# Kernel tuning notes

Hardware: AMD Instinct MI355X
Metric: run time of the kernel (lower is better)

Reference implementation:

```python
import jax, jax.numpy as jnp
import numpy as np

B, T, K = 512, 1024, 48


def setup_inputs() -> dict:
    key = jax.random.key(0)
    k1, k2, k3, k4, k5, k6 = jax.random.split(key, 6)
    return {
        "emission_scores": jax.random.normal(k1, (B, T, K), dtype=jnp.float32),
        "lengths": jax.random.randint(k2, (B,), 1, T + 1, dtype=jnp.int64),
        "tags": jax.random.randint(k3, (B, T), 0, K, dtype=jnp.int64),
        "prior": 0.1 * jax.random.normal(k4, (K,), dtype=jnp.float32),
        "transition": 0.1 * jax.random.normal(k5, (K, K), dtype=jnp.float32),
        "final_transition": 0.1 * jax.random.normal(k6, (K,), dtype=jnp.float32),
    }


def _partition_function(emission_scores, lengths, prior, transition, final_transition):
    batch, timesteps, num_tags = emission_scores.shape
    # alpha_0[b, i] = emis[b, 0, i] + prior[i]
    alpha0 = emission_scores[:, 0, :] + prior[None, :]

    def step(prev_alpha, emis_t):
        # alpha_t[b, i] = logsumexp_j(prev_alpha[b, j] + transition[i, j]) + emis_t[b, i]
        a = jax.nn.logsumexp(prev_alpha[:, None, :] + transition[None, :, :], axis=2)
        a = a + emis_t
        return a, a

    emis_rest = jnp.swapaxes(emission_scores, 0, 1)[1:]  # [T-1, B, K]
    _, alphas = jax.lax.scan(step, alpha0, emis_rest)
    alphas = jnp.concatenate([alpha0[None], alphas], axis=0)  # [T, B, K]
    alpha_final = alphas[lengths - 1, jnp.arange(batch)]  # [B, K] at last valid step
    alpha_final = alpha_final + final_transition[None, :]
    return jax.nn.logsumexp(alpha_final, axis=1)


def _score_path(emission_scores, lengths, tags, prior, transition, final_transition):
    batch, timesteps, num_tags = emission_scores.shape
    emis_tag = jnp.take_along_axis(emission_scores, tags[:, :, None], axis=2)[..., 0]  # [B, T]
    trans = transition[tags[:, 1:], tags[:, :-1]]  # [B, T-1]
    pr = prior[tags[:, 0]][:, None]  # [B, 1]
    scores = jnp.concatenate([pr, trans], axis=1) + emis_tag  # [B, T]
    valid = jnp.arange(timesteps)[None, :] < lengths[:, None]  # True for t < length
    scores = jnp.where(valid, scores, 0.0)
    final_tags = tags[jnp.arange(batch), lengths - 1]
    return jnp.sum(scores, axis=1) + final_transition[final_tags]


def reference(emission_scores, lengths, tags, prior, transition, final_transition):
    lengths = jnp.clip(lengths, 1, None)
    logZ = _partition_function(emission_scores, lengths, prior, transition, final_transition)
    path = _score_path(emission_scores, lengths, tags, prior, transition, final_transition)
    return jnp.mean(logZ - path)
```

## Files before the change

### kernel.cpp

```cpp
#include <hip/hip_runtime.h>


#define BB    512
#define TT    1024
#define KK    48
#define GG    16
#define NGRP  32
#define NSLOT 16
#define SLOTB 4096
#define PHASE 8
#define NPROD 4
#define BLKT  (64 * (1 + NPROD))

typedef __attribute__((ext_vector_type(4))) short bf16x4;
typedef __attribute__((ext_vector_type(4))) float f32x4;

__device__ __forceinline__ f32x4 mfma16(bf16x4 a, bf16x4 b, f32x4 c) {
#if __has_builtin(__builtin_amdgcn_mfma_f32_16x16x16bf16_1k)
    return __builtin_amdgcn_mfma_f32_16x16x16bf16_1k(a, b, c, 0, 0, 0);
#else
    f32x4 d;
    asm volatile("v_mfma_f32_16x16x16_bf16 %0, %1, %2, %3"
                 : "=v"(d) : "v"(a), "v"(b), "v"(c));
    return d;
#endif
}

__device__ __forceinline__ unsigned pk2(float lo, float hi) {
    return __builtin_amdgcn_perm(__float_as_uint(hi) + 0x8000u,
                                 __float_as_uint(lo) + 0x8000u,
                                 0x07060302u);
}
__device__ __forceinline__ bf16x4 pack4(float a, float b, float c, float d) {
    union { unsigned u[2]; bf16x4 v; } x;
    x.u[0] = pk2(a, b);
    x.u[1] = pk2(c, d);
    return x.v;
}

__device__ __forceinline__ float wave_reduce_sum(float v) {
    #pragma unroll
    for (int off = 32; off > 0; off >>= 1)
        v += __shfl_xor(v, off, 64);
    return v;
}

__device__ __forceinline__ void load_lds16(const float* g, void* l) {
    __builtin_amdgcn_global_load_lds(
        (const __attribute__((address_space(1))) unsigned int*)g,
        (__attribute__((address_space(3))) unsigned int*)l,
        16, 0, 0);
}

__global__ __launch_bounds__(BLKT, 1) void crf_main_kernel(
    const float* __restrict__ emis,
    const int*   __restrict__ lengths,
    const int*   __restrict__ tags,
    const float* __restrict__ prior,
    const float* __restrict__ trans,
    const float* __restrict__ finalT,
    float*       __restrict__ ws)
{
    __shared__ __align__(16) unsigned char ring[NSLOT * SLOTB];

    const int tid  = threadIdx.x;
    const int wv   = tid >> 6;
    const int lane = tid & 63;

    if (blockIdx.x >= NGRP) {
        const int b = blockIdx.x - NGRP;
        int len = lengths[b];
        len = (len < 1) ? 1 : (len > TT ? TT : len);
        const float* eb = emis + (size_t)b * TT * KK;
        const int*   tg = tags + (size_t)b * TT;
        float ps = 0.0f;
        for (int t = tid; t < len; t += BLKT) {
            int cur = tg[t];
            float ev = eb[(size_t)t * KK + cur];
            float tr = (t == 0) ? prior[cur] : trans[cur * KK + tg[t - 1]];
            ps += ev + tr;
        }
        ps = wave_reduce_sum(ps);
        float* red = (float*)ring;
        if (lane == 0) red[wv] = ps;
        __syncthreads();
        if (tid == 0) {
            float s = red[0];
            #pragma unroll
            for (int j = 1; j <= NPROD; ++j) s += red[j];
            ws[BB + b] = s + finalT[tg[len - 1]];
        }
        return;
    }

    const int g = blockIdx.x;

    int myLen = lengths[g * GG + (lane & 15)];
    myLen = (myLen < 1) ? 1 : (myLen > TT ? TT : myLen);
    int gmax = myLen;
    #pragma unroll
    for (int off = 32; off > 0; off >>= 1) {
        int o = __shfl_xor(gmax, off, 64);
        gmax = (o > gmax) ? o : gmax;
    }
    const int nsteps = gmax - 1;
    const int nphase = (nsteps + PHASE - 1) / PHASE;

    if (wv >= 1) {
        const float* base[4];
        #pragma unroll
        for (int j = 0; j < 4; ++j) {
            int s  = j * 4 + (lane >> 4);
            int kg = (lane & 15) ^ s;
            if (kg >= 12) kg = 0;
            base[j] = emis + ((size_t)(g * GG + s) * TT) * KK + kg * 4;
        }
        for (int k = 0; k < nphase; ++k) {
            int t0 = 1 + k * PHASE + (wv - 1);
            #pragma unroll
            for (int h = 0; h < 2; ++h) {
                int t  = t0 + 4 * h;
                int tc = (t > nsteps) ? nsteps : t;
                unsigned char* lp = &ring[(t & (NSLOT - 1)) * SLOTB];
                #pragma unroll
                for (int j = 0; j < 4; ++j)
                    load_lds16(base[j] + (size_t)tc * KK, lp + j * 1024);
            }
            __syncthreads();
        }
        return;
    }

    const int col   = lane & 15;
    const int grp   = lane >> 4;
    const int rbase = grp * 4;
    const int seq   = g * GG + col;
    const int lenn1 = myLen - 1;

    bf16x4 A[3][3];
    #pragma unroll
    for (int mt = 0; mt < 3; ++mt) {
        #pragma unroll
        for (int kt = 0; kt < 3; ++kt) {
            float4 tv = *reinterpret_cast<const float4*>(
                trans + (size_t)(mt * 16 + col) * KK + kt * 16 + rbase);
            A[mt][kt] = pack4(__expf(tv.x), __expf(tv.y),
                              __expf(tv.z), __expf(tv.w));
        }
    }

    float expF[12];
    #pragma unroll
    for (int mt = 0; mt < 3; ++mt) {
        float4 fv = *reinterpret_cast<const float4*>(finalT + mt * 16 + rbase);
        expF[mt*4+0] = __expf(fv.x); expF[mt*4+1] = __expf(fv.y);
        expF[mt*4+2] = __expf(fv.z); expF[mt*4+3] = __expf(fv.w);
    }

    const float* ebase = emis + (size_t)seq * TT * KK + rbase;

    float w[12];
    float c;
    float zcap = 0.0f;
    {
        float a0[12];
        #pragma unroll
        for (int mt = 0; mt < 3; ++mt) {
            float4 ev = *reinterpret_cast<const float4*>(ebase + mt * 16);
            float4 pv = *reinterpret_cast<const float4*>(prior + mt * 16 + rbase);
            a0[mt*4+0] = ev.x + pv.x;
            a0[mt*4+1] = ev.y + pv.y;
            a0[mt*4+2] = ev.z + pv.z;
            a0[mt*4+3] = ev.w + pv.w;
        }
        float mx = a0[0];
        #pragma unroll
        for (int r = 1; r < 12; ++r) mx = fmaxf(mx, a0[r]);
        mx = fmaxf(mx, __shfl_xor(mx, 16, 64));
        mx = fmaxf(mx, __shfl_xor(mx, 32, 64));
        c = mx;
        #pragma unroll
        for (int r = 0; r < 12; ++r) w[r] = __expf(a0[r] - c);
        if (__ballot(lenn1 == 0)) {
            float S = 0.0f;
            #pragma unroll
            for (int r = 0; r < 12; ++r) S = fmaf(w[r], expF[r], S);
            S += __shfl_xor(S, 16, 64);
            S += __shfl_xor(S, 32, 64);
            if (lenn1 == 0) zcap = c + __logf(S);
        }
    }

    bf16x4 Bt[3];
    Bt[0] = pack4(w[0], w[1], w[2],  w[3]);
    Bt[1] = pack4(w[4], w[5], w[6],  w[7]);
    Bt[2] = pack4(w[8], w[9], w[10], w[11]);

    int loff[3];
    #pragma unroll
    for (int mt = 0; mt < 3; ++mt)
        loff[mt] = col * 256 + (((mt * 4 + grp) ^ col) << 4);

    const f32x4 zero4 = {0.f, 0.f, 0.f, 0.f};
    for (int k = 0; k < nphase; ++k) {
        __syncthreads();
        #pragma unroll
        for (int s8 = 0; s8 < PHASE; ++s8) {
            const int t = 1 + k * PHASE + s8;
            const unsigned char* sp = &ring[(t & (NSLOT - 1)) * SLOTB];
            float4 E0 = *reinterpret_cast<const float4*>(sp + loff[0]);
            float4 E1 = *reinterpret_cast<const float4*>(sp + loff[1]);
            float4 E2 = *reinterpret_cast<const float4*>(sp + loff[2]);

            f32x4 D0 = mfma16(A[0][0], Bt[0], zero4);
            f32x4 D1 = mfma16(A[1][0], Bt[0], zero4);
            f32x4 D2 = mfma16(A[2][0], Bt[0], zero4);
            D0 = mfma16(A[0][1], Bt[1], D0);
            D1 = mfma16(A[1][1], Bt[1], D1);
            D2 = mfma16(A[2][1], Bt[1], D2);
            D0 = mfma16(A[0][2], Bt[2], D0);
            D1 = mfma16(A[1][2], Bt[2], D1);
            D2 = mfma16(A[2][2], Bt[2], D2);

            w[0]  = D0.x * __expf(E0.x);
            w[1]  = D0.y * __expf(E0.y);
            w[2]  = D0.z * __expf(E0.z);
            w[3]  = D0.w * __expf(E0.w);
            w[4]  = D1.x * __expf(E1.x);
            w[5]  = D1.y * __expf(E1.y);
            w[6]  = D1.z * __expf(E1.z);
            w[7]  = D1.w * __expf(E1.w);
            w[8]  = D2.x * __expf(E2.x);
            w[9]  = D2.y * __expf(E2.y);
            w[10] = D2.z * __expf(E2.z);
            w[11] = D2.w * __expf(E2.w);

            if ((t & 7) == 0) {
                float mx = w[0];
                #pragma unroll
                for (int r = 1; r < 12; ++r) mx = fmaxf(mx, w[r]);
                mx = fmaxf(mx, __shfl_xor(mx, 16, 64));
                mx = fmaxf(mx, __shfl_xor(mx, 32, 64));
                c += __logf(mx);
                float rm = __builtin_amdgcn_rcpf(mx);
                #pragma unroll
                for (int r = 0; r < 12; ++r) w[r] *= rm;
            }

            if (__ballot(t == lenn1)) {
                float S = 0.0f;
                #pragma unroll
                for (int r = 0; r < 12; ++r) S = fmaf(w[r], expF[r], S);
                S += __shfl_xor(S, 16, 64);
                S += __shfl_xor(S, 32, 64);
                if (t == lenn1) zcap = c + __logf(S);
            }

            Bt[0] = pack4(w[0], w[1], w[2],  w[3]);
            Bt[1] = pack4(w[4], w[5], w[6],  w[7]);
            Bt[2] = pack4(w[8], w[9], w[10], w[11]);
        }
    }

    if (lane < GG) ws[seq] = zcap;
}

__global__ __launch_bounds__(512) void reduce_mean_kernel(
    const float* __restrict__ ws, float* __restrict__ out)
{
    __shared__ float sm[8];
    int tid = threadIdx.x;
    float x = ws[tid] - ws[BB + tid];
    x = wave_reduce_sum(x);
    if ((tid & 63) == 0) sm[tid >> 6] = x;
    __syncthreads();
    if (tid < 8) {
        float y = sm[tid];
        y += __shfl_xor(y, 1, 64);
        y += __shfl_xor(y, 2, 64);
        y += __shfl_xor(y, 4, 64);
        if (tid == 0) out[0] = y * (1.0f / 512.0f);
    }
}

extern "C" void kernel_launch(void* const* d_in, const int* in_sizes, int n_in,
                              void* d_out, int out_size, void* d_ws, size_t ws_size,
                              hipStream_t stream) {
    const float* emis    = (const float*)d_in[0];
    const int*   lengths = (const int*)  d_in[1];
    const int*   tags    = (const int*)  d_in[2];
    const float* prior   = (const float*)d_in[3];
    const float* trans   = (const float*)d_in[4];
    const float* finalT  = (const float*)d_in[5];

    float* ws  = (float*)d_ws;
    float* out = (float*)d_out;

    crf_main_kernel<<<NGRP + BB, BLKT, 0, stream>>>(emis, lengths, tags, prior,
                                                    trans, finalT, ws);
    reduce_mean_kernel<<<1, 512, 0, stream>>>(ws, out);
}
```

Before: 341.2 us.

## Replace barrier-synced LDS ring with flag-based producer/consumer and producer-side exp

Producer waves now load emissions into registers, apply exp, and write the pre-exponentiated values into a compact LDS ring. Block-wide __syncthreads is replaced by per-producer and consumer counters in LDS polled with s_sleep, so the serial consumer wave no longer waits at barriers. The consumer's per-step exp work moves to the producers. Producers drop from 4 to 3 and bf16 packing uses the hardware cvt_pk_bf16 builtin where available. The cost is spin-wait polling and correctness that depends on LDS memory ordering without barriers.

Measured after the change: 331.6 us. 1.03x faster.

```diff
diff --git a/kernel.cpp b/kernel.cpp
--- a/kernel.cpp
+++ b/kernel.cpp
@@ -7,10 +7,10 @@
 #define GG    16
 #define NGRP  32
 #define NSLOT 16
-#define SLOTB 4096
+#define SLOTB (KK * GG * 4)
 #define PHASE 8
-#define NPROD 4
-#define BLKT  (64 * (1 + NPROD))
+#define NPROD 3
+#define BLKT  256
 
 typedef __attribute__((ext_vector_type(4))) short bf16x4;
 typedef __attribute__((ext_vector_type(4))) float f32x4;
@@ -26,11 +26,20 @@
 #endif
 }
 
+#if __has_builtin(__builtin_amdgcn_cvt_pk_bf16_f32)
+typedef __attribute__((ext_vector_type(2))) __bf16 bf16x2_v;
+__device__ __forceinline__ unsigned pk2(float lo, float hi) {
+    union { bf16x2_v v; unsigned u; } x;
+    x.v = __builtin_amdgcn_cvt_pk_bf16_f32(lo, hi);
+    return x.u;
+}
+#else
 __device__ __forceinline__ unsigned pk2(float lo, float hi) {
     return __builtin_amdgcn_perm(__float_as_uint(hi) + 0x8000u,
                                  __float_as_uint(lo) + 0x8000u,
                                  0x07060302u);
 }
+#endif
 __device__ __forceinline__ bf16x4 pack4(float a, float b, float c, float d) {
     union { unsigned u[2]; bf16x4 v; } x;
     x.u[0] = pk2(a, b);
@@ -43,13 +52,6 @@
     for (int off = 32; off > 0; off >>= 1)
         v += __shfl_xor(v, off, 64);
     return v;
-}
-
-__device__ __forceinline__ void load_lds16(const float* g, void* l) {
-    __builtin_amdgcn_global_load_lds(
-        (const __attribute__((address_space(1))) unsigned int*)g,
-        (__attribute__((address_space(3))) unsigned int*)l,
-        16, 0, 0);
 }
 
 __global__ __launch_bounds__(BLKT, 1) void crf_main_kernel(
@@ -62,6 +64,8 @@
     float*       __restrict__ ws)
 {
     __shared__ __align__(16) unsigned char ring[NSLOT * SLOTB];
+    __shared__ int prodCnt[NPROD];
+    __shared__ int consCnt;
 
     const int tid  = threadIdx.x;
     const int wv   = tid >> 6;
@@ -84,16 +88,17 @@
         float* red = (float*)ring;
         if (lane == 0) red[wv] = ps;
         __syncthreads();
-        if (tid == 0) {
-            float s = red[0];
-            #pragma unroll
-            for (int j = 1; j <= NPROD; ++j) s += red[j];
-            ws[BB + b] = s + finalT[tg[len - 1]];
-        }
+        if (tid == 0)
+            ws[BB + b] = red[0] + red[1] + red[2] + red[3] + finalT[tg[len - 1]];
         return;
     }
 
     const int g = blockIdx.x;
+
+    if (tid == 0) {
+        prodCnt[0] = 0; prodCnt[1] = 0; prodCnt[2] = 0; consCnt = 0;
+    }
+    __syncthreads();
 
     int myLen = lengths[g * GG + (lane & 15)];
     myLen = (myLen < 1) ? 1 : (myLen > TT ? TT : myLen);
@@ -107,27 +112,60 @@
     const int nphase = (nsteps + PHASE - 1) / PHASE;
 
     if (wv >= 1) {
-        const float* base[4];
-        #pragma unroll
-        for (int j = 0; j < 4; ++j) {
-            int s  = j * 4 + (lane >> 4);
-            int kg = (lane & 15) ^ s;
-            if (kg >= 12) kg = 0;
-            base[j] = emis + ((size_t)(g * GG + s) * TT) * KK + kg * 4;
-        }
+        size_t go[3]; int lo16[3];
+        #pragma unroll
+        for (int j = 0; j < 3; ++j) {
+            int idx = lane + 64 * j;
+            int s   = idx / 12;
+            int kg  = idx - s * 12;
+            go[j]   = (size_t)(g * GG + s) * (TT * KK) + kg * 4;
+            lo16[j] = idx * 16;
+        }
+        const int sA = wv - 1;
+        float4 L[9];
+
+#define PLOAD(KP)                                                          \
+        {                                                                  \
+            _Pragma("unroll")                                              \
+            for (int h = 0; h < 3; ++h) {                                  \
+                int s = sA + 3 * h;                                        \
+                if (s < PHASE) {                                           \
+                    int t  = 1 + (KP) * PHASE + s;                         \
+                    int tc = (t > nsteps) ? nsteps : t;                    \
+                    _Pragma("unroll")                                      \
+                    for (int j = 0; j < 3; ++j)                            \
+                        L[h*3+j] = *reinterpret_cast<const float4*>(       \
+                            emis + go[j] + (size_t)tc * KK);               \
+                }                                                          \
+            }                                                              \
+        }
+
+        PLOAD(0);
+        volatile int* vc = &consCnt;
         for (int k = 0; k < nphase; ++k) {
-            int t0 = 1 + k * PHASE + (wv - 1);
+            while (*vc < k - 1) __builtin_amdgcn_s_sleep(1);
+            asm volatile("" ::: "memory");
             #pragma unroll
-            for (int h = 0; h < 2; ++h) {
-                int t  = t0 + 4 * h;
-                int tc = (t > nsteps) ? nsteps : t;
-                unsigned char* lp = &ring[(t & (NSLOT - 1)) * SLOTB];
-                #pragma unroll
-                for (int j = 0; j < 4; ++j)
-                    load_lds16(base[j] + (size_t)tc * KK, lp + j * 1024);
+            for (int h = 0; h < 3; ++h) {
+                int s = sA + 3 * h;
+                if (s < PHASE) {
+                    int t = 1 + k * PHASE + s;
+                    unsigned char* bp = &ring[(t & (NSLOT - 1)) * SLOTB];
+                    #pragma unroll
+                    for (int j = 0; j < 3; ++j) {
+                        float4 l = L[h*3+j];
+                        float4 e;
+                        e.x = __expf(l.x); e.y = __expf(l.y);
+                        e.z = __expf(l.z); e.w = __expf(l.w);
+                        *reinterpret_cast<float4*>(bp + lo16[j]) = e;
+                    }
+                }
             }
-            __syncthreads();
-        }
+            __threadfence_block();
+            if (lane == 0) *(volatile int*)&prodCnt[sA] = k + 1;
+            PLOAD(k + 1);
+        }
+#undef PLOAD
         return;
     }
 
@@ -196,21 +234,22 @@
     Bt[1] = pack4(w[4], w[5], w[6],  w[7]);
     Bt[2] = pack4(w[8], w[9], w[10], w[11]);
 
-    int loff[3];
-    #pragma unroll
-    for (int mt = 0; mt < 3; ++mt)
-        loff[mt] = col * 256 + (((mt * 4 + grp) ^ col) << 4);
-
+    const int foff = col * 48 + grp * 4;
     const f32x4 zero4 = {0.f, 0.f, 0.f, 0.f};
+    volatile int* vp = prodCnt;
+
     for (int k = 0; k < nphase; ++k) {
-        __syncthreads();
+        while (vp[0] < k + 1 || vp[1] < k + 1 || vp[2] < k + 1)
+            __builtin_amdgcn_s_sleep(1);
+        asm volatile("" ::: "memory");
         #pragma unroll
         for (int s8 = 0; s8 < PHASE; ++s8) {
             const int t = 1 + k * PHASE + s8;
-            const unsigned char* sp = &ring[(t & (NSLOT - 1)) * SLOTB];
-            float4 E0 = *reinterpret_cast<const float4*>(sp + loff[0]);
-            float4 E1 = *reinterpret_cast<const float4*>(sp + loff[1]);
-            float4 E2 = *reinterpret_cast<const float4*>(sp + loff[2]);
+            const float* sp = reinterpret_cast<const float*>(
+                &ring[(t & (NSLOT - 1)) * SLOTB]) + foff;
+            float4 X0 = *reinterpret_cast<const float4*>(sp);
+            float4 X1 = *reinterpret_cast<const float4*>(sp + 16);
+            float4 X2 = *reinterpret_cast<const float4*>(sp + 32);
 
             f32x4 D0 = mfma16(A[0][0], Bt[0], zero4);
             f32x4 D1 = mfma16(A[1][0], Bt[0], zero4);
@@ -222,18 +261,12 @@
             D1 = mfma16(A[1][2], Bt[2], D1);
             D2 = mfma16(A[2][2], Bt[2], D2);
 
-            w[0]  = D0.x * __expf(E0.x);
-            w[1]  = D0.y * __expf(E0.y);
-            w[2]  = D0.z * __expf(E0.z);
-            w[3]  = D0.w * __expf(E0.w);
-            w[4]  = D1.x * __expf(E1.x);
-            w[5]  = D1.y * __expf(E1.y);
-            w[6]  = D1.z * __expf(E1.z);
-            w[7]  = D1.w * __expf(E1.w);
-            w[8]  = D2.x * __expf(E2.x);
-            w[9]  = D2.y * __expf(E2.y);
-            w[10] = D2.z * __expf(E2.z);
-            w[11] = D2.w * __expf(E2.w);
+            w[0]  = D0.x * X0.x;  w[1]  = D0.y * X0.y;
+            w[2]  = D0.z * X0.z;  w[3]  = D0.w * X0.w;
+            w[4]  = D1.x * X1.x;  w[5]  = D1.y * X1.y;
+            w[6]  = D1.z * X1.z;  w[7]  = D1.w * X1.w;
+            w[8]  = D2.x * X2.x;  w[9]  = D2.y * X2.y;
+            w[10] = D2.z * X2.z;  w[11] = D2.w * X2.w;
 
             if ((t & 7) == 0) {
                 float mx = w[0];
@@ -260,6 +293,9 @@
             Bt[1] = pack4(w[4], w[5], w[6],  w[7]);
             Bt[2] = pack4(w[8], w[9], w[10], w[11]);
         }
+        __threadfence_block();
+        asm volatile("" ::: "memory");
+        if (lane == 0) *(volatile int*)&consCnt = k + 1;
     }
 
     if (lane < GG) ws[seq] = zcap;
```
